# Kernel tuning notes

Hardware: AMD Instinct MI355X
Metric: run time of the kernel (lower is better)

Reference implementation:

```python
import jax, jax.numpy as jnp
import numpy as np

N = 20000      # nodes
E = 400000     # edges
D = 256        # input_dim == hidden_dim
L = 4          # num_layers
EIN = 32       # edgenet_input_dim // 2
EH = 128       # edge parser hidden
NC = 2         # num_classes
JK = L * D     # 1024
BN_EPS = 1e-5


def setup_inputs() -> dict:
    key = jax.random.key(0)
    ks = jax.random.split(key, 16)
    s = 0.05
    inp = {
        "features": jax.random.normal(ks[0], (N, D), jnp.float32),
        "edge_index": jax.random.randint(ks[1], (2, E), 0, N, dtype=jnp.int64),
        "edgenet_input": jax.random.normal(ks[2], (E, 2 * EIN), jnp.float32),
        # ChebConv weights: [layer, k, in, out] (all layers 256->256, K=3, no bias)
        "cheb_w": jax.random.normal(ks[3], (L, 3, D, D), jnp.float32) * s,
        # EdgeEncoder (PAE-style) parser: Linear(32,128)+ReLU+BN+Linear(128,128)
        "en_w1": jax.random.normal(ks[4], (EIN, EH), jnp.float32) * s,
        "en_b1": jnp.zeros((EH,), jnp.float32),
        "en_g1": jnp.ones((EH,), jnp.float32),
        "en_be1": jnp.zeros((EH,), jnp.float32),
        "en_w2": jax.random.normal(ks[5], (EH, EH), jnp.float32) * s,
        "en_b2": jnp.zeros((EH,), jnp.float32),
        # cls head: Linear(1024,256)+ReLU+BN(256)+Linear(256,2)
        "cls_w1": jax.random.normal(ks[6], (JK, 256), jnp.float32) * s,
        "cls_b1": jnp.zeros((256,), jnp.float32),
        "cls_g": jnp.ones((256,), jnp.float32),
        "cls_b": jnp.zeros((256,), jnp.float32),
        "cls_w2": jax.random.normal(ks[7], (256, NC), jnp.float32) * s,
        "cls_b2": jnp.zeros((NC,), jnp.float32),
    }
    return inp


def _bn_eval(x, g, b):
    # eval-mode BatchNorm1d with fresh running stats (mean=0, var=1)
    return x * (g / jnp.sqrt(1.0 + BN_EPS)) + b


def reference(features, edge_index, edgenet_input, cheb_w,
              en_w1, en_b1, en_g1, en_be1, en_w2, en_b2,
              cls_w1, cls_b1, cls_g, cls_b, cls_w2, cls_b2):
    row, col = edge_index[0], edge_index[1]

    # ---- EdgeEncoder (PAE): shared parser on both halves + cosine sim ----
    def parser(x):
        h = jnp.maximum(x @ en_w1 + en_b1, 0.0)
        h = _bn_eval(h, en_g1, en_be1)
        return h @ en_w2 + en_b2

    half = edgenet_input.shape[1] // 2
    h1 = parser(edgenet_input[:, :half])
    h2 = parser(edgenet_input[:, half:])
    n1 = jnp.maximum(jnp.linalg.norm(h1, axis=1), 1e-8)
    n2 = jnp.maximum(jnp.linalg.norm(h2, axis=1), 1e-8)
    cos = jnp.sum(h1 * h2, axis=1) / (n1 * n2)
    edge_weight = (cos + 1.0) * 0.5  # [E]

    # ---- ChebConv sym normalization (lambda_max=2): L_hat = -D^-1/2 A D^-1/2 ----
    deg = jax.ops.segment_sum(edge_weight, row, num_segments=N)
    dis = jnp.where(deg > 0, jax.lax.rsqrt(jnp.maximum(deg, 1e-30)), 0.0)
    norm = -dis[row] * edge_weight * dis[col]  # [E]

    def prop(x):  # out[col] += norm * x[row]
        return jax.ops.segment_sum(x[row] * norm[:, None], col, num_segments=N)

    # ---- stacked ChebConv (K=3, no bias) + ReLU + JK concat ----
    x = features
    jk = None
    for i in range(L):
        W = cheb_w[i]
        Tx0 = x
        Tx1 = prop(Tx0)
        Tx2 = 2.0 * prop(Tx1) - Tx0
        h = jnp.maximum(Tx0 @ W[0] + Tx1 @ W[1] + Tx2 @ W[2], 0.0)
        jk = h if i == 0 else jnp.concatenate([jk, h], axis=1)
        x = h

    # ---- cls head ----
    z = jnp.maximum(jk @ cls_w1 + cls_b1, 0.0)
    z = _bn_eval(z, cls_g, cls_b)
    logit = z @ cls_w2 + cls_b2
    return (logit, edge_weight)
```

## Files before the change

kernel.cpp:

```cpp
#include <hip/hip_runtime.h>

#define NN 20000
#define EE 400000
#define RSBN 0.9999950000374997f

typedef __attribute__((ext_vector_type(8))) short short8;
typedef __attribute__((ext_vector_type(8))) unsigned short ushort8;
typedef __attribute__((ext_vector_type(4))) float floatx4;

__device__ __forceinline__ short f2bf(float f) {
  union { float f; unsigned u; } v; v.f = f;
  unsigned r = v.u + 0x7fffu + ((v.u >> 16) & 1u);
  return (short)(r >> 16);
}
__device__ __forceinline__ float bf2f(unsigned short u) {
  union { unsigned u; float f; } v; v.u = ((unsigned)u) << 16;
  return v.f;
}
__device__ __forceinline__ void gl_lds16(const void* g, void* l) {
  __builtin_amdgcn_global_load_lds(
      (const __attribute__((address_space(1))) unsigned*)g,
      (__attribute__((address_space(3))) unsigned*)l, 16, 0, 0);
}

__global__ __launch_bounds__(256) void ewconv_kernel(
    const float* __restrict__ w1, const float* __restrict__ w2,
    unsigned short* __restrict__ ewf)
{
  int tid = threadIdx.x;
#pragma unroll
  for (int i = 0; i < 16; i++) {
    int idx = i * 256 + tid;
    int k = idx >> 7, n = idx & 127;
    int pos = ((n >> 4) * 64 + (k >> 3) * 16 + (n & 15)) * 8 + (k & 7);
    ewf[pos] = f2bf(w1[idx]);
  }
#pragma unroll
  for (int i = 0; i < 64; i++) {
    int idx = i * 256 + tid;
    int k = idx >> 7, n = idx & 127;
    int pos = (((k >> 5) * 8 + (n >> 4)) * 64 + ((k >> 3) & 3) * 16 + (n & 15)) * 8 + (k & 7);
    ewf[4096 + pos] = f2bf(w2[idx]);
  }
}

#define ASP 136
__global__ __launch_bounds__(512, 4) void edge_kernel(
    const float* __restrict__ xin, const int* __restrict__ eidx,
    const unsigned short* __restrict__ ewf,
    const float* __restrict__ b1, const float* __restrict__ g1,
    const float* __restrict__ be1, const float* __restrict__ b2,
    float* __restrict__ ew_out, float* __restrict__ ew_ws,
    float* __restrict__ deg, int* __restrict__ cnt)
{
  __shared__ short wbuf[20480];
  __shared__ short as_s[128 * ASP];

  int tid = threadIdx.x;
  int lane = tid & 63;
  int wv = tid >> 6;
  int l15 = lane & 15;
  int quad = lane >> 4;

#pragma unroll
  for (int i = 0; i < 5; i++)
    gl_lds16(ewf + (i * 512 + tid) * 8, &wbuf[(i * 512 + tid) * 8]);

  const short* w1f = wbuf;
  const short* w2f = wbuf + 4096;

  float b1j[8], s1j[8], be1j[8], b2j[8];
#pragma unroll
  for (int c = 0; c < 8; c++) {
    int n = c * 16 + l15;
    b1j[c] = b1[n]; s1j[c] = g1[n] * RSBN; be1j[c] = be1[n]; b2j[c] = b2[n];
  }

  int rowbase = blockIdx.x * 128 + wv * 16;

  short8 af;
  {
    const float* xp = xin + (size_t)(rowbase + l15) * 32 + quad * 8;
    float4 v0 = *(const float4*)xp;
    float4 v1 = *(const float4*)(xp + 4);
    af[0] = f2bf(v0.x); af[1] = f2bf(v0.y); af[2] = f2bf(v0.z); af[3] = f2bf(v0.w);
    af[4] = f2bf(v1.x); af[5] = f2bf(v1.y); af[6] = f2bf(v1.z); af[7] = f2bf(v1.w);
  }

  __syncthreads();

  floatx4 acc[8];
#pragma unroll
  for (int c = 0; c < 8; c++) {
    floatx4 z = {0.f, 0.f, 0.f, 0.f};
    acc[c] = __builtin_amdgcn_mfma_f32_16x16x32_bf16(
        af, *(const short8*)&w1f[(c * 64 + lane) * 8], z, 0, 0, 0);
  }

#pragma unroll
  for (int c = 0; c < 8; c++)
#pragma unroll
    for (int r = 0; r < 4; r++) {
      float a = fmaxf(acc[c][r] + b1j[c], 0.f) * s1j[c] + be1j[c];
      as_s[(wv * 16 + quad * 4 + r) * ASP + c * 16 + l15] = f2bf(a);
    }

  floatx4 acc2[8];
#pragma unroll
  for (int c = 0; c < 8; c++) acc2[c] = (floatx4){0.f, 0.f, 0.f, 0.f};
#pragma unroll
  for (int s = 0; s < 4; s++) {
    short8 a2 = *(const short8*)&as_s[(wv * 16 + l15) * ASP + s * 32 + quad * 8];
#pragma unroll
    for (int c = 0; c < 8; c++) {
      short8 bf = *(const short8*)&w2f[((s * 8 + c) * 64 + lane) * 8];
      acc2[c] = __builtin_amdgcn_mfma_f32_16x16x32_bf16(a2, bf, acc2[c], 0, 0, 0);
    }
  }

  float p[2], qq[2], rr[2];
#pragma unroll
  for (int i = 0; i < 2; i++) { p[i] = 0.f; qq[i] = 0.f; rr[i] = 0.f; }
#pragma unroll
  for (int c = 0; c < 8; c++)
#pragma unroll
    for (int i = 0; i < 2; i++) {
      float hx = acc2[c][2 * i]     + b2j[c];
      float hy = acc2[c][2 * i + 1] + b2j[c];
      p[i]  += hx * hy;
      qq[i] += hx * hx;
      rr[i] += hy * hy;
    }
#pragma unroll
  for (int m = 1; m < 16; m <<= 1)
#pragma unroll
    for (int i = 0; i < 2; i++) {
      p[i]  += __shfl_xor(p[i], m, 64);
      qq[i] += __shfl_xor(qq[i], m, 64);
      rr[i] += __shfl_xor(rr[i], m, 64);
    }
  if (l15 == 0) {
#pragma unroll
    for (int i = 0; i < 2; i++) {
      int row = rowbase + quad * 4 + 2 * i;
      int e = row >> 1;
      float n1 = fmaxf(sqrtf(qq[i]), 1e-8f);
      float n2 = fmaxf(sqrtf(rr[i]), 1e-8f);
      float w = (p[i] / (n1 * n2) + 1.f) * 0.5f;
      ew_out[e] = w;
      ew_ws[e] = w;
      atomicAdd(deg + eidx[e], w);
      atomicAdd(cnt + eidx[EE + e], 1);
    }
  }
}

__global__ __launch_bounds__(256) void fconv_kernel(const float* __restrict__ src,
                                                    unsigned short* __restrict__ dst) {
  size_t i = ((size_t)blockIdx.x * 256 + threadIdx.x) * 8;
  float4 a = *(const float4*)(src + i);
  float4 b = *(const float4*)(src + i + 4);
  ushort8 o;
  o[0] = f2bf(a.x); o[1] = f2bf(a.y); o[2] = f2bf(a.z); o[3] = f2bf(a.w);
  o[4] = f2bf(b.x); o[5] = f2bf(b.y); o[6] = f2bf(b.z); o[7] = f2bf(b.w);
  *(ushort8*)(dst + i) = o;
}

__global__ __launch_bounds__(256) void wconv_kernel(
    const float* __restrict__ cheb_w, const float* __restrict__ cls_w1,
    unsigned short* __restrict__ wtc, unsigned short* __restrict__ clsT)
{
  __shared__ unsigned short tile[64][80];
  int z = blockIdx.z;
  const float* src; unsigned short* dst; int ldk;
  if (z < 12) {
    int l = z / 3, c = z % 3;
    src = cheb_w + (size_t)z * 65536;
    dst = wtc + (size_t)l * 196608 + c * 256;
    ldk = 768;
  } else {
    int c = z - 12;
    src = cls_w1 + (size_t)c * 65536;
    dst = clsT + c * 256;
    ldk = 1024;
  }
  int t = threadIdx.x;
  int k0 = blockIdx.x * 64, n0 = blockIdx.y * 64;
#pragma unroll
  for (int pass = 0; pass < 4; pass++) {
    int kk = pass * 16 + (t >> 4);
    int nl = (t & 15) * 4;
    float4 v = *(const float4*)(src + (size_t)(k0 + kk) * 256 + n0 + nl);
    tile[nl + 0][kk] = f2bf(v.x);
    tile[nl + 1][kk] = f2bf(v.y);
    tile[nl + 2][kk] = f2bf(v.z);
    tile[nl + 3][kk] = f2bf(v.w);
  }
  __syncthreads();
  int nl = t >> 2, kc = (t & 3) * 16;
  ushort8 v0 = *(const ushort8*)&tile[nl][kc];
  ushort8 v1 = *(const ushort8*)&tile[nl][kc + 8];
  unsigned short* dp = dst + (size_t)(n0 + nl) * ldk + k0 + kc;
  *(ushort8*)dp = v0;
  *(ushort8*)(dp + 8) = v1;
}

__global__ void dis_kernel(const float* __restrict__ deg, float* __restrict__ dis) {
  int i = blockIdx.x * 256 + threadIdx.x;
  if (i < NN) {
    float d = deg[i];
    dis[i] = d > 0.f ? 1.f / sqrtf(fmaxf(d, 1e-30f)) : 0.f;
  }
}

__global__ __launch_bounds__(1024) void scan_kernel(const int* __restrict__ cnt, int* __restrict__ ptr) {
  __shared__ int sums[1024];
  int tid = threadIdx.x;
  const int n = NN;
  const int chunk = (n + 1023) / 1024;
  int base = tid * chunk;
  int s = 0;
  for (int i = 0; i < chunk; i++) { int idx = base + i; if (idx < n) s += cnt[idx]; }
  sums[tid] = s;
  __syncthreads();
  for (int off = 1; off < 1024; off <<= 1) {
    int v = (tid >= off) ? sums[tid - off] : 0;
    __syncthreads();
    sums[tid] += v;
    __syncthreads();
  }
  int run = (tid == 0) ? 0 : sums[tid - 1];
  for (int i = 0; i < chunk; i++) {
    int idx = base + i;
    if (idx < n) { ptr[idx] = run; run += cnt[idx]; }
  }
  if (tid == 1023) ptr[n] = run;
}

__global__ void fill_kernel(const int* __restrict__ eidx, const float* __restrict__ ew,
                            const float* __restrict__ dis, const int* __restrict__ ptr,
                            int* __restrict__ fill, int* __restrict__ cidx, float* __restrict__ cval) {
  int e = blockIdx.x * 256 + threadIdx.x;
  if (e < EE) {
    int r = eidx[e], c = eidx[EE + e];
    float nv = -dis[r] * ew[e] * dis[c];
    int pos = ptr[c] + atomicAdd(&fill[c], 1);
    cidx[pos] = r;
    cval[pos] = nv;
  }
}

__global__ __launch_bounds__(256) void prop_kernel(
    const unsigned short* __restrict__ x, int ldx,
    const int* __restrict__ cidx, const float* __restrict__ cval,
    const int* __restrict__ ptr,
    unsigned short* __restrict__ y, int ldy,
    float alpha, const unsigned short* __restrict__ sub, int ldsub)
{
  int c = blockIdx.x * 8 + (threadIdx.x >> 5);
  int lane5 = threadIdx.x & 31;
  int d = lane5 * 8;
  int p0 = ptr[c], p1 = ptr[c + 1];
  float a[8] = {0.f, 0.f, 0.f, 0.f, 0.f, 0.f, 0.f, 0.f};
  int p = p0;
  for (; p + 3 < p1; p += 4) {
    int r0 = cidx[p], r1 = cidx[p + 1], r2 = cidx[p + 2], r3 = cidx[p + 3];
    float w0 = cval[p], w1v = cval[p + 1], w2v = cval[p + 2], w3v = cval[p + 3];
    ushort8 v0 = *(const ushort8*)(x + (size_t)r0 * ldx + d);
    ushort8 v1 = *(const ushort8*)(x + (size_t)r1 * ldx + d);
    ushort8 v2 = *(const ushort8*)(x + (size_t)r2 * ldx + d);
    ushort8 v3 = *(const ushort8*)(x + (size_t)r3 * ldx + d);
#pragma unroll
    for (int j = 0; j < 8; j++)
      a[j] += w0 * bf2f(v0[j]) + w1v * bf2f(v1[j]) + w2v * bf2f(v2[j]) + w3v * bf2f(v3[j]);
  }
  for (; p < p1; p++) {
    int r0 = cidx[p]; float w0 = cval[p];
    ushort8 v0 = *(const ushort8*)(x + (size_t)r0 * ldx + d);
#pragma unroll
    for (int j = 0; j < 8; j++) a[j] += w0 * bf2f(v0[j]);
  }
  ushort8 o;
  if (sub) {
    ushort8 sv = *(const ushort8*)(sub + (size_t)c * ldsub + d);
#pragma unroll
    for (int j = 0; j < 8; j++) o[j] = f2bf(alpha * a[j] - bf2f(sv[j]));
  } else {
#pragma unroll
    for (int j = 0; j < 8; j++) o[j] = f2bf(a[j]);
  }
  *(ushort8*)(y + (size_t)c * ldy + d) = o;
}

__global__ __launch_bounds__(256, 2) void mgemm_kernel(
    const unsigned short* A0, const unsigned short* A1,
    const unsigned short* A2, const unsigned short* A3,
    int l0, int l1, int l2, int l3, int nchunks,
    const unsigned short* __restrict__ BT, int ldbt,
    unsigned short* __restrict__ Cb, float* __restrict__ Cf, int ldc, int M,
    const float* __restrict__ bias, const float* __restrict__ bng,
    const float* __restrict__ bnb)
{
  __shared__ short As[4 * 64 * 8];
  __shared__ short Bs[4 * 128 * 8];
  int tid = threadIdx.x;
  int lane = tid & 63;
  int wv = tid >> 6;
  int l15 = lane & 15, quad = lane >> 4;
  int wr = wv >> 1, wc = wv & 1;
  int m0 = blockIdx.x * 64, n0 = blockIdx.y * 128;

  const unsigned short* Ap[4] = {A0, A1, A2, A3};
  int Al[4] = {l0, l1, l2, l3};

  int arow = tid & 63, ac = tid >> 6;
  int brow = tid & 127, bc = tid >> 7;

  floatx4 acc[2][4];
#pragma unroll
  for (int mi = 0; mi < 2; mi++)
#pragma unroll
    for (int nj = 0; nj < 4; nj++) acc[mi][nj] = (floatx4){0.f, 0.f, 0.f, 0.f};

  for (int c = 0; c < nchunks; c++) {
    const unsigned short* Abase = Ap[c] + (size_t)(m0 + arow) * Al[c] + ac * 8;
    const unsigned short* Bbase = BT + (size_t)(n0 + brow) * ldbt + c * 256 + bc * 8;
#pragma unroll 1
    for (int kb = 0; kb < 256; kb += 32) {
      __syncthreads();
      gl_lds16(Abase + kb, &As[tid * 8]);
      gl_lds16(Bbase + kb, &Bs[tid * 8]);
      gl_lds16(Bbase + 16 + kb, &Bs[(tid + 256) * 8]);
      __syncthreads();
      short8 af[2], bfv[4];
#pragma unroll
      for (int mi = 0; mi < 2; mi++)
        af[mi] = *(const short8*)&As[(quad * 64 + wr * 32 + mi * 16 + l15) * 8];
#pragma unroll
      for (int nj = 0; nj < 4; nj++)
        bfv[nj] = *(const short8*)&Bs[(quad * 128 + wc * 64 + nj * 16 + l15) * 8];
#pragma unroll
      for (int nj = 0; nj < 4; nj++)
#pragma unroll
        for (int mi = 0; mi < 2; mi++)
          acc[mi][nj] = __builtin_amdgcn_mfma_f32_16x16x32_bf16(af[mi], bfv[nj], acc[mi][nj], 0, 0, 0);
    }
  }

  if (Cb) {
#pragma unroll
    for (int mi = 0; mi < 2; mi++)
#pragma unroll
      for (int r = 0; r < 4; r++) {
        int row = m0 + wr * 32 + mi * 16 + quad * 4 + r;
        if (row < M) {
#pragma unroll
          for (int nj = 0; nj < 4; nj++) {
            int col = n0 + wc * 64 + nj * 16 + l15;
            Cb[(size_t)row * ldc + col] = (unsigned short)f2bf(fmaxf(acc[mi][nj][r], 0.f));
          }
        }
      }
  } else {
    float bs[4], g[4], bb[4];
#pragma unroll
    for (int nj = 0; nj < 4; nj++) {
      int col = n0 + wc * 64 + nj * 16 + l15;
      bs[nj] = bias[col]; g[nj] = bng[col] * RSBN; bb[nj] = bnb[col];
    }
#pragma unroll
    for (int mi = 0; mi < 2; mi++)
#pragma unroll
      for (int r = 0; r < 4; r++) {
        int row = m0 + wr * 32 + mi * 16 + quad * 4 + r;
        if (row < M) {
#pragma unroll
          for (int nj = 0; nj < 4; nj++) {
            int col = n0 + wc * 64 + nj * 16 + l15;
            float v = fmaxf(acc[mi][nj][r] + bs[nj], 0.f) * g[nj] + bb[nj];
            Cf[(size_t)row * ldc + col] = v;
          }
        }
      }
  }
}

__global__ __launch_bounds__(256) void logit_kernel(
    const float* __restrict__ z, const float* __restrict__ w2,
    const float* __restrict__ b2, float* __restrict__ out)
{
  int node = blockIdx.x * 4 + (threadIdx.x >> 6);
  if (node >= NN) return;
  int lane = threadIdx.x & 63;
  int k = lane * 4;
  float4 zv = *(const float4*)(z + (size_t)node * 256 + k);
  float4 wa = *(const float4*)(w2 + k * 2);
  float4 wb = *(const float4*)(w2 + k * 2 + 4);
  float a0 = zv.x * wa.x + zv.y * wa.z + zv.z * wb.x + zv.w * wb.z;
  float a1 = zv.x * wa.y + zv.y * wa.w + zv.z * wb.y + zv.w * wb.w;
#pragma unroll
  for (int m = 32; m >= 1; m >>= 1) {
    a0 += __shfl_xor(a0, m, 64);
    a1 += __shfl_xor(a1, m, 64);
  }
  if (lane == 0) {
    out[(size_t)node * 2]     = a0 + b2[0];
    out[(size_t)node * 2 + 1] = a1 + b2[1];
  }
}

extern "C" void kernel_launch(void* const* d_in, const int* in_sizes, int n_in,
                              void* d_out, int out_size, void* d_ws, size_t ws_size,
                              hipStream_t stream) {
  const float* features = (const float*)d_in[0];
  const int*   eidx     = (const int*)d_in[1];
  const float* xin      = (const float*)d_in[2];
  const float* cheb_w   = (const float*)d_in[3];
  const float* en_w1    = (const float*)d_in[4];
  const float* en_b1    = (const float*)d_in[5];
  const float* en_g1    = (const float*)d_in[6];
  const float* en_be1   = (const float*)d_in[7];
  const float* en_w2    = (const float*)d_in[8];
  const float* en_b2    = (const float*)d_in[9];
  const float* cls_w1   = (const float*)d_in[10];
  const float* cls_b1   = (const float*)d_in[11];
  const float* cls_g    = (const float*)d_in[12];
  const float* cls_b    = (const float*)d_in[13];
  const float* cls_w2   = (const float*)d_in[14];
  const float* cls_b2   = (const float*)d_in[15];
  float* out = (float*)d_out;

  char* ws = (char*)d_ws;
  size_t off = 0;
  auto alloc = [&](size_t bytes) -> void* {
    void* p = ws + off;
    off += (bytes + 255) & ~(size_t)255;
    return p;
  };
  float* deg  = (float*)alloc((size_t)NN * 4);
  int*   cnt  = (int*)  alloc((size_t)NN * 4);
  int*   fil  = (int*)  alloc((size_t)NN * 4);
  size_t zero_len = off;
  float* dis  = (float*)alloc((size_t)NN * 4);
  int*   ptr  = (int*)  alloc((size_t)(NN + 1) * 4);
  float* ew   = (float*)alloc((size_t)EE * 4);
  int*   cidx = (int*)  alloc((size_t)EE * 4);
  float* cval = (float*)alloc((size_t)EE * 4);
  unsigned short* featb = (unsigned short*)alloc((size_t)NN * 256 * 2);
  unsigned short* Tx1   = (unsigned short*)alloc((size_t)NN * 256 * 2);
  unsigned short* Tx2   = (unsigned short*)alloc((size_t)NN * 256 * 2);
  unsigned short* jk    = (unsigned short*)alloc((size_t)NN * 1024 * 2);
  float* zbuf = (float*)alloc((size_t)NN * 256 * 4);
  unsigned short* wtc   = (unsigned short*)alloc((size_t)4 * 196608 * 2);
  unsigned short* clsT  = (unsigned short*)alloc((size_t)256 * 1024 * 2);
  unsigned short* ewf   = (unsigned short*)alloc((size_t)20480 * 2);
  alloc(262144);

  hipMemsetAsync(deg, 0, zero_len, stream);

  ewconv_kernel<<<1, 256, 0, stream>>>(en_w1, en_w2, ewf);
  edge_kernel<<<6250, 512, 0, stream>>>(xin, eidx, ewf, en_b1, en_g1, en_be1, en_b2,
                                        out + (size_t)NN * 2, ew, deg, cnt);
  fconv_kernel<<<2500, 256, 0, stream>>>(features, featb);
  wconv_kernel<<<dim3(4, 4, 16), 256, 0, stream>>>(cheb_w, cls_w1, wtc, clsT);
  dis_kernel<<<(NN + 255) / 256, 256, 0, stream>>>(deg, dis);
  scan_kernel<<<1, 1024, 0, stream>>>(cnt, ptr);
  fill_kernel<<<(EE + 255) / 256, 256, 0, stream>>>(eidx, ew, dis, ptr, fil, cidx, cval);

  dim3 ggrid(313, 2);
  for (int i = 0; i < 4; i++) {
    const unsigned short* x = (i == 0) ? featb : (jk + (size_t)(i - 1) * 256);
    int ldx = (i == 0) ? 256 : 1024;
    prop_kernel<<<2500, 256, 0, stream>>>(x, ldx, cidx, cval, ptr, Tx1, 256, 1.f, nullptr, 0);
    prop_kernel<<<2500, 256, 0, stream>>>(Tx1, 256, cidx, cval, ptr, Tx2, 256, 2.f, x, ldx);
    mgemm_kernel<<<ggrid, 256, 0, stream>>>(x, Tx1, Tx2, nullptr, ldx, 256, 256, 0, 3,
                                            wtc + (size_t)i * 196608, 768,
                                            jk + (size_t)i * 256, nullptr, 1024, NN,
                                            nullptr, nullptr, nullptr);
  }

  mgemm_kernel<<<ggrid, 256, 0, stream>>>(jk, jk + 256, jk + 512, jk + 768,
                                          1024, 1024, 1024, 1024, 4, clsT, 1024,
                                          nullptr, zbuf, 256, NN,
                                          cls_b1, cls_g, cls_b);
  logit_kernel<<<NN / 4, 256, 0, stream>>>(zbuf, cls_w2, cls_b2, out);
}
```

Baseline: 693.4 us.

## Fold BN into parser weights, pad CSR rows to four, pack bf16 conversions

The eval-mode BatchNorm scale and shift are folded into the second parser layer's weights and bias, and both biases are injected through the MFMA accumulator initializers. This removes per-element bias/BN arithmetic and per-thread parameter loads in the edge kernel. CSR rows are padded to multiples of four with zero-filled entries, so the propagation loop can use vector int4/float4 index and value loads and needs no remainder loop. It also drops the duplicate edge-weight workspace write in favour of the output buffer, and uses packed bf16x2 conversions. The cost is a larger memset over the padded CSR arrays and more gathers on padding entries, which all point at row 0 with weight zero.

```diff
diff --git a/kernel.cpp b/kernel.cpp
--- a/kernel.cpp
+++ b/kernel.cpp
@@ -1,4 +1,5 @@
 #include <hip/hip_runtime.h>
+#include <hip/hip_bf16.h>
 
 #define NN 20000
 #define EE 400000
@@ -13,6 +14,11 @@
   unsigned r = v.u + 0x7fffu + ((v.u >> 16) & 1u);
   return (short)(r >> 16);
 }
+__device__ __forceinline__ unsigned f2bf2(float x, float y) {
+  union { __hip_bfloat162 h; unsigned u; } v;
+  v.h = __float22bfloat162_rn(make_float2(x, y));
+  return v.u;
+}
 __device__ __forceinline__ float bf2f(unsigned short u) {
   union { unsigned u; float f; } v; v.u = ((unsigned)u) << 16;
   return v.f;
@@ -25,6 +31,8 @@
 
 __global__ __launch_bounds__(256) void ewconv_kernel(
     const float* __restrict__ w1, const float* __restrict__ w2,
+    const float* __restrict__ g1, const float* __restrict__ be1,
+    const float* __restrict__ b1, const float* __restrict__ b2,
     unsigned short* __restrict__ ewf)
 {
   int tid = threadIdx.x;
@@ -40,7 +48,14 @@
     int idx = i * 256 + tid;
     int k = idx >> 7, n = idx & 127;
     int pos = (((k >> 5) * 8 + (n >> 4)) * 64 + ((k >> 3) & 3) * 16 + (n & 15)) * 8 + (k & 7);
-    ewf[4096 + pos] = f2bf(w2[idx]);
+    ewf[4096 + pos] = f2bf(w2[idx] * g1[k] * RSBN);
+  }
+  float* fb = (float*)(ewf + 20480);
+  if (tid < 128) {
+    fb[tid] = b1[tid];
+    float acc = b2[tid];
+    for (int k = 0; k < 128; k++) acc += be1[k] * w2[k * 128 + tid] * g1[k] * RSBN;
+    fb[128 + tid] = acc;
   }
 }
 
@@ -48,12 +63,10 @@
 __global__ __launch_bounds__(512, 4) void edge_kernel(
     const float* __restrict__ xin, const int* __restrict__ eidx,
     const unsigned short* __restrict__ ewf,
-    const float* __restrict__ b1, const float* __restrict__ g1,
-    const float* __restrict__ be1, const float* __restrict__ b2,
-    float* __restrict__ ew_out, float* __restrict__ ew_ws,
+    float* __restrict__ ew_out,
     float* __restrict__ deg, int* __restrict__ cnt)
 {
-  __shared__ short wbuf[20480];
+  __shared__ short wbuf[20992];
   __shared__ short as_s[128 * ASP];
 
   int tid = threadIdx.x;
@@ -65,16 +78,11 @@
 #pragma unroll
   for (int i = 0; i < 5; i++)
     gl_lds16(ewf + (i * 512 + tid) * 8, &wbuf[(i * 512 + tid) * 8]);
+  if (tid < 64)
+    gl_lds16(ewf + (2560 + tid) * 8, &wbuf[(2560 + tid) * 8]);
 
   const short* w1f = wbuf;
   const short* w2f = wbuf + 4096;
-
-  float b1j[8], s1j[8], be1j[8], b2j[8];
-#pragma unroll
-  for (int c = 0; c < 8; c++) {
-    int n = c * 16 + l15;
-    b1j[c] = b1[n]; s1j[c] = g1[n] * RSBN; be1j[c] = be1[n]; b2j[c] = b2[n];
-  }
 
   int rowbase = blockIdx.x * 128 + wv * 16;
 
@@ -83,16 +91,26 @@
     const float* xp = xin + (size_t)(rowbase + l15) * 32 + quad * 8;
     float4 v0 = *(const float4*)xp;
     float4 v1 = *(const float4*)(xp + 4);
-    af[0] = f2bf(v0.x); af[1] = f2bf(v0.y); af[2] = f2bf(v0.z); af[3] = f2bf(v0.w);
-    af[4] = f2bf(v1.x); af[5] = f2bf(v1.y); af[6] = f2bf(v1.z); af[7] = f2bf(v1.w);
+    union { short8 s; unsigned u[4]; } a;
+    a.u[0] = f2bf2(v0.x, v0.y); a.u[1] = f2bf2(v0.z, v0.w);
+    a.u[2] = f2bf2(v1.x, v1.y); a.u[3] = f2bf2(v1.z, v1.w);
+    af = a.s;
   }
 
   __syncthreads();
 
+  const float* fb = (const float*)(wbuf + 20480);
+  float b1j[8], b2j[8];
+#pragma unroll
+  for (int c = 0; c < 8; c++) {
+    b1j[c] = fb[c * 16 + l15];
+    b2j[c] = fb[128 + c * 16 + l15];
+  }
+
   floatx4 acc[8];
 #pragma unroll
   for (int c = 0; c < 8; c++) {
-    floatx4 z = {0.f, 0.f, 0.f, 0.f};
+    floatx4 z = {b1j[c], b1j[c], b1j[c], b1j[c]};
     acc[c] = __builtin_amdgcn_mfma_f32_16x16x32_bf16(
         af, *(const short8*)&w1f[(c * 64 + lane) * 8], z, 0, 0, 0);
   }
@@ -100,14 +118,16 @@
 #pragma unroll
   for (int c = 0; c < 8; c++)
 #pragma unroll
-    for (int r = 0; r < 4; r++) {
-      float a = fmaxf(acc[c][r] + b1j[c], 0.f) * s1j[c] + be1j[c];
-      as_s[(wv * 16 + quad * 4 + r) * ASP + c * 16 + l15] = f2bf(a);
+    for (int r = 0; r < 4; r += 2) {
+      unsigned pk = f2bf2(fmaxf(acc[c][r], 0.f), fmaxf(acc[c][r + 1], 0.f));
+      int base = (wv * 16 + quad * 4 + r) * ASP + c * 16 + l15;
+      as_s[base] = (short)(pk & 0xffff);
+      as_s[base + ASP] = (short)(pk >> 16);
     }
 
   floatx4 acc2[8];
 #pragma unroll
-  for (int c = 0; c < 8; c++) acc2[c] = (floatx4){0.f, 0.f, 0.f, 0.f};
+  for (int c = 0; c < 8; c++) acc2[c] = (floatx4){b2j[c], b2j[c], b2j[c], b2j[c]};
 #pragma unroll
   for (int s = 0; s < 4; s++) {
     short8 a2 = *(const short8*)&as_s[(wv * 16 + l15) * ASP + s * 32 + quad * 8];
@@ -125,8 +145,8 @@
   for (int c = 0; c < 8; c++)
 #pragma unroll
     for (int i = 0; i < 2; i++) {
-      float hx = acc2[c][2 * i]     + b2j[c];
-      float hy = acc2[c][2 * i + 1] + b2j[c];
+      float hx = acc2[c][2 * i];
+      float hy = acc2[c][2 * i + 1];
       p[i]  += hx * hy;
       qq[i] += hx * hx;
       rr[i] += hy * hy;
@@ -148,7 +168,6 @@
       float n2 = fmaxf(sqrtf(rr[i]), 1e-8f);
       float w = (p[i] / (n1 * n2) + 1.f) * 0.5f;
       ew_out[e] = w;
-      ew_ws[e] = w;
       atomicAdd(deg + eidx[e], w);
       atomicAdd(cnt + eidx[EE + e], 1);
     }
@@ -160,10 +179,10 @@
   size_t i = ((size_t)blockIdx.x * 256 + threadIdx.x) * 8;
   float4 a = *(const float4*)(src + i);
   float4 b = *(const float4*)(src + i + 4);
-  ushort8 o;
-  o[0] = f2bf(a.x); o[1] = f2bf(a.y); o[2] = f2bf(a.z); o[3] = f2bf(a.w);
-  o[4] = f2bf(b.x); o[5] = f2bf(b.y); o[6] = f2bf(b.z); o[7] = f2bf(b.w);
-  *(ushort8*)(dst + i) = o;
+  union { ushort8 s; unsigned u[4]; } o;
+  o.u[0] = f2bf2(a.x, a.y); o.u[1] = f2bf2(a.z, a.w);
+  o.u[2] = f2bf2(b.x, b.y); o.u[3] = f2bf2(b.z, b.w);
+  *(ushort8*)(dst + i) = o.s;
 }
 
 __global__ __launch_bounds__(256) void wconv_kernel(
@@ -220,7 +239,10 @@
   const int chunk = (n + 1023) / 1024;
   int base = tid * chunk;
   int s = 0;
-  for (int i = 0; i < chunk; i++) { int idx = base + i; if (idx < n) s += cnt[idx]; }
+  for (int i = 0; i < chunk; i++) {
+    int idx = base + i;
+    if (idx < n) s += (cnt[idx] + 3) & ~3;
+  }
   sums[tid] = s;
   __syncthreads();
   for (int off = 1; off < 1024; off <<= 1) {
@@ -232,7 +254,7 @@
   int run = (tid == 0) ? 0 : sums[tid - 1];
   for (int i = 0; i < chunk; i++) {
     int idx = base + i;
-    if (idx < n) { ptr[idx] = run; run += cnt[idx]; }
+    if (idx < n) { ptr[idx] = run; run += (cnt[idx] + 3) & ~3; }
   }
   if (tid == 1023) ptr[n] = run;
 }
@@ -262,34 +284,29 @@
   int d = lane5 * 8;
   int p0 = ptr[c], p1 = ptr[c + 1];
   float a[8] = {0.f, 0.f, 0.f, 0.f, 0.f, 0.f, 0.f, 0.f};
-  int p = p0;
-  for (; p + 3 < p1; p += 4) {
-    int r0 = cidx[p], r1 = cidx[p + 1], r2 = cidx[p + 2], r3 = cidx[p + 3];
-    float w0 = cval[p], w1v = cval[p + 1], w2v = cval[p + 2], w3v = cval[p + 3];
-    ushort8 v0 = *(const ushort8*)(x + (size_t)r0 * ldx + d);
-    ushort8 v1 = *(const ushort8*)(x + (size_t)r1 * ldx + d);
-    ushort8 v2 = *(const ushort8*)(x + (size_t)r2 * ldx + d);
-    ushort8 v3 = *(const ushort8*)(x + (size_t)r3 * ldx + d);
+  for (int p = p0; p < p1; p += 4) {
+    int4 r4 = *(const int4*)(cidx + p);
+    float4 w4 = *(const float4*)(cval + p);
+    ushort8 v0 = *(const ushort8*)(x + (size_t)r4.x * ldx + d);
+    ushort8 v1 = *(const ushort8*)(x + (size_t)r4.y * ldx + d);
+    ushort8 v2 = *(const ushort8*)(x + (size_t)r4.z * ldx + d);
+    ushort8 v3 = *(const ushort8*)(x + (size_t)r4.w * ldx + d);
 #pragma unroll
     for (int j = 0; j < 8; j++)
-      a[j] += w0 * bf2f(v0[j]) + w1v * bf2f(v1[j]) + w2v * bf2f(v2[j]) + w3v * bf2f(v3[j]);
-  }
-  for (; p < p1; p++) {
-    int r0 = cidx[p]; float w0 = cval[p];
-    ushort8 v0 = *(const ushort8*)(x + (size_t)r0 * ldx + d);
-#pragma unroll
-    for (int j = 0; j < 8; j++) a[j] += w0 * bf2f(v0[j]);
-  }
-  ushort8 o;
+      a[j] += w4.x * bf2f(v0[j]) + w4.y * bf2f(v1[j]) + w4.z * bf2f(v2[j]) + w4.w * bf2f(v3[j]);
+  }
+  union { ushort8 s; unsigned u[4]; } o;
   if (sub) {
     ushort8 sv = *(const ushort8*)(sub + (size_t)c * ldsub + d);
 #pragma unroll
-    for (int j = 0; j < 8; j++) o[j] = f2bf(alpha * a[j] - bf2f(sv[j]));
+    for (int j = 0; j < 8; j += 2)
+      o.u[j >> 1] = f2bf2(alpha * a[j] - bf2f(sv[j]), alpha * a[j + 1] - bf2f(sv[j + 1]));
   } else {
 #pragma unroll
-    for (int j = 0; j < 8; j++) o[j] = f2bf(a[j]);
-  }
-  *(ushort8*)(y + (size_t)c * ldy + d) = o;
+    for (int j = 0; j < 8; j += 2)
+      o.u[j >> 1] = f2bf2(a[j], a[j + 1]);
+  }
+  *(ushort8*)(y + (size_t)c * ldy + d) = o.s;
 }
 
 __global__ __launch_bounds__(256, 2) void mgemm_kernel(
@@ -437,15 +454,15 @@
     off += (bytes + 255) & ~(size_t)255;
     return p;
   };
+  const int CSRN = EE + 4 * NN;
   float* deg  = (float*)alloc((size_t)NN * 4);
   int*   cnt  = (int*)  alloc((size_t)NN * 4);
   int*   fil  = (int*)  alloc((size_t)NN * 4);
+  float* cval = (float*)alloc((size_t)CSRN * 4);
+  int*   cidx = (int*)  alloc((size_t)CSRN * 4);
   size_t zero_len = off;
   float* dis  = (float*)alloc((size_t)NN * 4);
   int*   ptr  = (int*)  alloc((size_t)(NN + 1) * 4);
-  float* ew   = (float*)alloc((size_t)EE * 4);
-  int*   cidx = (int*)  alloc((size_t)EE * 4);
-  float* cval = (float*)alloc((size_t)EE * 4);
   unsigned short* featb = (unsigned short*)alloc((size_t)NN * 256 * 2);
   unsigned short* Tx1   = (unsigned short*)alloc((size_t)NN * 256 * 2);
   unsigned short* Tx2   = (unsigned short*)alloc((size_t)NN * 256 * 2);
@@ -453,14 +470,15 @@
   float* zbuf = (float*)alloc((size_t)NN * 256 * 4);
   unsigned short* wtc   = (unsigned short*)alloc((size_t)4 * 196608 * 2);
   unsigned short* clsT  = (unsigned short*)alloc((size_t)256 * 1024 * 2);
-  unsigned short* ewf   = (unsigned short*)alloc((size_t)20480 * 2);
+  unsigned short* ewf   = (unsigned short*)alloc((size_t)20992 * 2);
   alloc(262144);
 
+  float* ew = out + (size_t)NN * 2;
+
   hipMemsetAsync(deg, 0, zero_len, stream);
 
-  ewconv_kernel<<<1, 256, 0, stream>>>(en_w1, en_w2, ewf);
-  edge_kernel<<<6250, 512, 0, stream>>>(xin, eidx, ewf, en_b1, en_g1, en_be1, en_b2,
-                                        out + (size_t)NN * 2, ew, deg, cnt);
+  ewconv_kernel<<<1, 256, 0, stream>>>(en_w1, en_w2, en_g1, en_be1, en_b1, en_b2, ewf);
+  edge_kernel<<<6250, 512, 0, stream>>>(xin, eidx, ewf, ew, deg, cnt);
   fconv_kernel<<<2500, 256, 0, stream>>>(features, featb);
   wconv_kernel<<<dim3(4, 4, 16), 256, 0, stream>>>(cheb_w, cls_w1, wtc, clsT);
   dis_kernel<<<(NN + 255) / 256, 256, 0, stream>>>(deg, dis);
```

After: 687.1 us. No clear change (-0.9%).
